# Optimization experiments

Hardware: AMD Instinct MI355X
Metric: run time of the kernel (lower is better)

The kernel has to match this reference:

```python
import jax, jax.numpy as jnp
import numpy as np

N = 100000      # nodes
E = 1000000     # edges (before self-loops)
IN_DIM = 256
H = 4           # heads
C = 32          # out_dim per head
NEG_SLOPE = 0.2  # PyG GATConv default negative_slope


def setup_inputs() -> dict:
    key = jax.random.key(0)
    ks = jax.random.split(key, 6)
    x = jax.random.normal(ks[0], (N, IN_DIM), jnp.float32)
    W = jax.random.normal(ks[1], (IN_DIM, H * C), jnp.float32) * (1.0 / np.sqrt(IN_DIM))
    a_src = jax.random.normal(ks[2], (H, C), jnp.float32) * 0.1
    a_dst = jax.random.normal(ks[3], (H, C), jnp.float32) * 0.1
    bias = jnp.zeros((H * C,), jnp.float32)
    edge_index = jax.random.randint(ks[4], (2, E), 0, N, dtype=jnp.int32)
    return {"x": x, "W": W, "a_src": a_src, "a_dst": a_dst, "bias": bias,
            "edge_index": edge_index}


def reference(x, W, a_src, a_dst, bias, edge_index):
    n = x.shape[0]
    # PyG GATConv default: add self-loops
    loops = jnp.arange(n, dtype=edge_index.dtype)
    src = jnp.concatenate([edge_index[0], loops])  # [E+N]
    dst = jnp.concatenate([edge_index[1], loops])  # [E+N]
    # linear transform -> [N, H, C]
    h = (x @ W).reshape(n, H, C)
    # per-node attention logits
    alpha_s = jnp.einsum('nhc,hc->nh', h, a_src)  # [N, H]
    alpha_d = jnp.einsum('nhc,hc->nh', h, a_dst)  # [N, H]
    # per-edge score, LeakyReLU
    e = jax.nn.leaky_relu(alpha_s[src] + alpha_d[dst], NEG_SLOPE)  # [E+N, H]
    # segment softmax over incoming edges of each destination node
    m = jax.lax.stop_gradient(jax.ops.segment_max(e, dst, num_segments=n))
    p = jnp.exp(e - m[dst])
    s = jax.ops.segment_sum(p, dst, num_segments=n)
    alpha = p / (s[dst] + 1e-16)  # [E+N, H]
    # weighted scatter-add of source features
    out = jax.ops.segment_sum(alpha[:, :, None] * h[src], dst, num_segments=n)  # [N, H, C]
    out = out.reshape(n, H * C) + bias
    return jnp.tanh(out)
```

## Files before the change

### kernel.cpp

```cpp
#include <hip/hip_runtime.h>

#define IN_DIM 256
#define HC     128
#define NHEAD  4
#define NEG    0.2f
#define BKT    1024
#define NBMAX  128
#define EPT2   8
#define BE     4096
#define PACKB  16

typedef __attribute__((ext_vector_type(8))) short short8v;
typedef __attribute__((ext_vector_type(4))) float f32x4;
typedef __attribute__((ext_vector_type(2))) float f32x2;
typedef __attribute__((ext_vector_type(4))) unsigned short ushort4v;

__device__ __forceinline__ unsigned short bf16_rn(float f) {
    unsigned u = __builtin_bit_cast(unsigned, f);
    return (unsigned short)((u + 0x7fffu + ((u >> 16) & 1u)) >> 16);
}
__device__ __forceinline__ float bf16_lo(unsigned v) {
    return __builtin_bit_cast(float, v << 16);
}
__device__ __forceinline__ float bf16_hi(unsigned v) {
    return __builtin_bit_cast(float, v & 0xffff0000u);
}
__device__ __forceinline__ float fast_tanh(float x) {
    float t = __expf(2.f * x);
    return fmaf(-2.f, __builtin_amdgcn_rcpf(t + 1.f), 1.f);
}
__device__ __forceinline__ float lrelu(float e) {
    return fmaxf(e, NEG * e);
}

__global__ __launch_bounds__(256) void pack_hist_kernel(const float* __restrict__ W,
                                                        unsigned short* __restrict__ w_hi,
                                                        const int* __restrict__ ei,
                                                        int* __restrict__ bucket_cnt,
                                                        int E, int nb) {
    __shared__ int lh[NBMAX];
    int tid = threadIdx.x;
    if (blockIdx.x < PACKB) {
        int t = blockIdx.x * 256 + tid;
        int l  = t & 63;
        int ct = (t >> 6) & 7;
        int s  = t >> 9;
        int kbase = s * 32 + (l >> 4) * 8;
        int col   = ct * 16 + (l & 15);
        size_t base = (size_t)t * 8;
#pragma unroll
        for (int e = 0; e < 8; ++e)
            w_hi[base + e] = bf16_rn(W[(size_t)(kbase + e) * HC + col]);
        return;
    }
    if (tid < NBMAX) lh[tid] = 0;
    __syncthreads();
    int base = (blockIdx.x - PACKB) * BE;
#pragma unroll
    for (int i = 0; i < 16; ++i) {
        int e = base + i * 256 + tid;
        if (e < E) atomicAdd(&lh[ei[E + e] >> 10], 1);
    }
    __syncthreads();
    if (tid < nb && lh[tid]) atomicAdd(&bucket_cnt[tid], lh[tid]);
}

__global__ __launch_bounds__(128) void bucket_scan_kernel(const int* __restrict__ bucket_cnt,
                                                          int* __restrict__ bucket_base,
                                                          int* __restrict__ bucket_cursor,
                                                          int nb) {
    __shared__ int ws0[1];
    int t = threadIdx.x;
    int v = (t < nb) ? bucket_cnt[t] : 0;
    int lane = t & 63, wd = t >> 6;
    int x = v;
#pragma unroll
    for (int off = 1; off < 64; off <<= 1) {
        int y = __shfl_up(x, off);
        if (lane >= off) x += y;
    }
    if (wd == 0 && lane == 63) ws0[0] = x;
    __syncthreads();
    int wo = wd ? ws0[0] : 0;
    int excl = wo + x - v;
    if (t < nb) { bucket_base[t] = excl; bucket_cursor[t] = excl; }
    if (t == 127) bucket_base[nb] = wo + x;
}

union KSmem {
    struct {
        unsigned short s_bf[64 * 256];
        float pS[64][4];
        float pD[64][4];
    } g;
    struct {
        int lh[NBMAX];
        int lofs[NBMAX];
        int gofs[NBMAX];
        int ws0;
        unsigned buf[BE];
    } s;
};

__global__ __launch_bounds__(512) void scatter_gemm_kernel(const int* __restrict__ ei,
                                                           int* __restrict__ bucket_cursor,
                                                           unsigned* __restrict__ bucket_data,
                                                           int E, int nb, int nblkE, int totalB,
                                                           const float* __restrict__ x,
                                                           const unsigned short* __restrict__ w_hi,
                                                           const float* __restrict__ a_src,
                                                           const float* __restrict__ a_dst,
                                                           unsigned short* __restrict__ h_bf,
                                                           float* __restrict__ alpha_s,
                                                           float* __restrict__ alpha_d, int n) {
    __shared__ KSmem sm;
    const int tid = threadIdx.x;
    const int bid = (int)blockIdx.x;

    const int s_before = (int)(((long long)bid * nblkE) / totalB);
    const bool is_scat = (int)(((long long)(bid + 1) * nblkE) / totalB) > s_before;

    if (is_scat) {
        if (tid < NBMAX) sm.s.lh[tid] = 0;
        __syncthreads();

        int base = s_before * BE;
        int bb[EPT2]; unsigned wv[EPT2]; int rr[EPT2];
#pragma unroll
        for (int i = 0; i < EPT2; ++i) {
            int e = base + i * 512 + tid;
            if (e < E) {
                int src = ei[e];
                int dst = ei[E + e];
                bb[i] = dst >> 10;
                wv[i] = (unsigned)src | ((unsigned)(dst & 1023) << 17);
                rr[i] = atomicAdd(&sm.s.lh[bb[i]], 1);
            } else bb[i] = -1;
        }
        __syncthreads();

        int lane = tid & 63, wd = tid >> 6;
        int v_ = 0, x_ = 0;
        if (tid < NBMAX) {
            v_ = sm.s.lh[tid]; x_ = v_;
#pragma unroll
            for (int off = 1; off < 64; off <<= 1) {
                int y = __shfl_up(x_, off);
                if (lane >= off) x_ += y;
            }
            if (wd == 0 && lane == 63) sm.s.ws0 = x_;
        }
        __syncthreads();
        if (tid < NBMAX) {
            int wo = wd ? sm.s.ws0 : 0;
            sm.s.lofs[tid] = wo + x_ - v_;
        }
        __syncthreads();

#pragma unroll
        for (int i = 0; i < EPT2; ++i)
            if (bb[i] >= 0) sm.s.buf[sm.s.lofs[bb[i]] + rr[i]] = wv[i];
        if (tid < nb) sm.s.gofs[tid] = sm.s.lh[tid] ? atomicAdd(&bucket_cursor[tid], sm.s.lh[tid]) : 0;
        __syncthreads();

        int wid = tid >> 6;
        for (int bk = wid; bk < nb; bk += 8) {
            int lo = sm.s.lofs[bk], cnt = sm.s.lh[bk], g = sm.s.gofs[bk];
            for (int j = lane; j < cnt; j += 64)
                bucket_data[g + j] = sm.s.buf[lo + j];
        }
        return;
    }

    const int gidx = bid - s_before;
    if (gidx * 64 >= n) return;
    const int l   = tid & 63;
    const int wv_ = tid >> 6;
    const int row0 = gidx * 64;

    const f32x4* x4 = reinterpret_cast<const f32x4*>(x);
#pragma unroll
    for (int i = 0; i < 8; ++i) {
        int row = i * 8 + wv_;
        int c4  = l;
        f32x4 v = (f32x4){0.f, 0.f, 0.f, 0.f};
        if (row0 + row < n) v = __builtin_nontemporal_load(&x4[(size_t)(row0 + row) * 64 + c4]);
        ushort4v b;
        b[0] = bf16_rn(v[0]); b[1] = bf16_rn(v[1]);
        b[2] = bf16_rn(v[2]); b[3] = bf16_rn(v[3]);
        int slot = (c4 >> 1) ^ (row & 7);
        int uidx = row * 256 + (slot << 3) + ((c4 & 1) << 2);
        *reinterpret_cast<ushort4v*>(&sm.g.s_bf[uidx]) = b;
    }
    __syncthreads();

    const int ct_g = wv_ & 3;
    const int rt_g = wv_ >> 2;
    const int rrow = l & 15;
    const int kq   = l >> 4;

    f32x4 acc[2][2];
#pragma unroll
    for (int a = 0; a < 2; ++a)
#pragma unroll
        for (int b = 0; b < 2; ++b) acc[a][b] = (f32x4){0.f, 0.f, 0.f, 0.f};

    for (int s = 0; s < 8; ++s) {
        short8v bh[2];
#pragma unroll
        for (int c = 0; c < 2; ++c) {
            int ct = ct_g * 2 + c;
            bh[c] = *reinterpret_cast<const short8v*>(w_hi + ((size_t)(s * 8 + ct) * 64 + l) * 8);
        }
#pragma unroll
        for (int r = 0; r < 2; ++r) {
            int arow = rt_g * 32 + r * 16 + rrow;
            int c16  = kq + s * 4;
            int uidx = arow * 256 + ((c16 ^ (arow & 7)) << 3);
            short8v ah = *reinterpret_cast<const short8v*>(&sm.g.s_bf[uidx]);
#pragma unroll
            for (int c = 0; c < 2; ++c)
                acc[r][c] = __builtin_amdgcn_mfma_f32_16x16x32_bf16(ah, bh[c], acc[r][c], 0, 0, 0);
        }
    }

#pragma unroll
    for (int r = 0; r < 2; ++r) {
#pragma unroll
        for (int c = 0; c < 2; ++c) {
            int col = (ct_g * 2 + c) * 16 + (l & 15);
#pragma unroll
            for (int q = 0; q < 4; ++q) {
                int row = row0 + rt_g * 32 + r * 16 + (l >> 4) * 4 + q;
                if (row < n) h_bf[(size_t)row * HC + col] = bf16_rn(acc[r][c][q]);
            }
        }
    }

    float asc[2], adc[2];
#pragma unroll
    for (int c = 0; c < 2; ++c) {
        int col = (ct_g * 2 + c) * 16 + (l & 15);
        asc[c] = a_src[col];
        adc[c] = a_dst[col];
    }
#pragma unroll
    for (int r = 0; r < 2; ++r) {
#pragma unroll
        for (int q = 0; q < 4; ++q) {
            float vS = acc[r][0][q] * asc[0] + acc[r][1][q] * asc[1];
            float vD = acc[r][0][q] * adc[0] + acc[r][1][q] * adc[1];
#pragma unroll
            for (int m = 1; m < 16; m <<= 1) {
                vS += __shfl_xor(vS, m);
                vD += __shfl_xor(vD, m);
            }
            if ((l & 15) == 0) {
                int rl = rt_g * 32 + r * 16 + (l >> 4) * 4 + q;
                sm.g.pS[rl][ct_g] = vS;
                sm.g.pD[rl][ct_g] = vD;
            }
        }
    }
    __syncthreads();
    if (tid < 256) {
        int rl = tid >> 2, h = tid & 3;
        int row = row0 + rl;
        if (row < n) {
            alpha_s[(size_t)row * 4 + h] = sm.g.pS[rl][h];
            alpha_d[(size_t)row * 4 + h] = sm.g.pD[rl][h];
        }
    }
}

__global__ __launch_bounds__(1024) void bucket_build_kernel(const int* __restrict__ bucket_base,
                                                            const unsigned* __restrict__ bucket_data,
                                                            int* __restrict__ deg,
                                                            int* __restrict__ row_start,
                                                            int* __restrict__ csr_src, int n) {
    __shared__ int lc[BKT];
    __shared__ int sc[BKT];
    __shared__ int wsum[16];

    int b = blockIdx.x;
    int base = bucket_base[b];
    int end  = bucket_base[b + 1];
    int t = threadIdx.x;

    lc[t] = 0;
    __syncthreads();
    for (int i = base + t; i < end; i += 1024)
        atomicAdd(&lc[__builtin_nontemporal_load(&bucket_data[i]) >> 17], 1);
    __syncthreads();

    int val = lc[t];
    int lane = t & 63, wd = t >> 6;
    int x = val;
#pragma unroll
    for (int off = 1; off < 64; off <<= 1) {
        int y = __shfl_up(x, off);
        if (lane >= off) x += y;
    }
    if (lane == 63) wsum[wd] = x;
    __syncthreads();
    if (wd == 0 && lane < 16) {
        int y = wsum[lane];
#pragma unroll
        for (int off = 1; off < 16; off <<= 1) {
            int z = __shfl_up(y, off);
            if (lane >= off) y += z;
        }
        wsum[lane] = y;
    }
    __syncthreads();
    int wo = wd ? wsum[wd - 1] : 0;
    int excl = wo + x - val;
    sc[t] = excl;
    int v = b * BKT + t;
    if (v < n) { deg[v] = val; row_start[v] = base + excl; }
    lc[t] = 0;
    __syncthreads();

    for (int i = base + t; i < end; i += 1024) {
        unsigned w = bucket_data[i];
        int d = w >> 17;
        int src = (int)(w & 0x1FFFFu);
        int p = atomicAdd(&lc[d], 1);
        csr_src[base + sc[d] + p] = src;
    }
}

__global__ __launch_bounds__(256, 4) void gather_kernel(const int* __restrict__ row_start,
                                                        const int* __restrict__ deg,
                                                        const int* __restrict__ csr_src,
                                                        const float* __restrict__ alpha_s,
                                                        const float* __restrict__ alpha_d,
                                                        const unsigned short* __restrict__ h_bf,
                                                        const float* __restrict__ bias,
                                                        float* __restrict__ out, int n) {
    int lane = threadIdx.x & 63;
    int wid  = threadIdx.x >> 6;
    int v = blockIdx.x * 4 + wid;
    if (v >= n) return;
    int start = row_start[v];
    int cnt = deg[v];
    int head = lane >> 4;
    int hc   = lane & 3;

    const unsigned* hb = reinterpret_cast<const unsigned*>(h_bf);

    float adC = alpha_d[(size_t)v * 4 + hc];
    float asC = alpha_s[(size_t)v * 4 + hc];
    float adH = __shfl(adC, head);
    float asH = __shfl(asC, head);
    float pself = __expf(lrelu(asH + adH));
    unsigned hv0 = hb[((unsigned)v << 6) + lane];
    float s = pself;
    float accx = pself * bf16_lo(hv0);
    float accy = pself * bf16_hi(hv0);

    int j = 0;
    for (; j + 8 <= cnt; j += 8) {
        int cv = csr_src[start + j + (lane & 7)];
        int sj = __shfl(cv, lane >> 2);
        float av = alpha_s[(size_t)sj * 4 + hc];
        float w  = __expf(lrelu(av + adC));
#pragma unroll
        for (int k = 0; k < 8; ++k) {
            int sk   = __shfl(cv, k);
            float wk = __shfl(w, (k << 2) | head);
            unsigned hk = hb[((unsigned)sk << 6) + lane];
            s += wk;
            accx = fmaf(wk, bf16_lo(hk), accx);
            accy = fmaf(wk, bf16_hi(hk), accy);
        }
    }
    if (j + 4 <= cnt) {
        int cv = csr_src[start + j + (lane & 3)];
        int sj = __shfl(cv, lane >> 2);
        float av = alpha_s[(size_t)sj * 4 + hc];
        float w  = __expf(lrelu(av + adC));
#pragma unroll
        for (int k = 0; k < 4; ++k) {
            int sk   = __shfl(cv, k);
            float wk = __shfl(w, (k << 2) | head);
            unsigned hk = hb[((unsigned)sk << 6) + lane];
            s += wk;
            accx = fmaf(wk, bf16_lo(hk), accx);
            accy = fmaf(wk, bf16_hi(hk), accy);
        }
        j += 4;
    }
    for (; j < cnt; ++j) {
        int s0 = csr_src[start + j];
        float a0 = alpha_s[(size_t)s0 * 4 + head];
        unsigned h0 = hb[((unsigned)s0 << 6) + lane];
        float w0 = __expf(lrelu(a0 + adH));
        s += w0;
        accx = fmaf(w0, bf16_lo(h0), accx);
        accy = fmaf(w0, bf16_hi(h0), accy);
    }

    float invH = __builtin_amdgcn_rcpf(s + 1e-16f);
    float2 b = reinterpret_cast<const float2*>(bias)[lane];
    f32x2 o;
    o[0] = fast_tanh(fmaf(accx, invH, b.x));
    o[1] = fast_tanh(fmaf(accy, invH, b.y));
    __builtin_nontemporal_store(o, &reinterpret_cast<f32x2*>(out)[(size_t)v * 64 + lane]);
}

extern "C" void kernel_launch(void* const* d_in, const int* in_sizes, int n_in,
                              void* d_out, int out_size, void* d_ws, size_t ws_size,
                              hipStream_t stream) {
    const float* x     = (const float*)d_in[0];
    const float* W     = (const float*)d_in[1];
    const float* a_src = (const float*)d_in[2];
    const float* a_dst = (const float*)d_in[3];
    const float* bias  = (const float*)d_in[4];
    const int*   ei    = (const int*)d_in[5];

    const int n = in_sizes[0] / IN_DIM;
    const int E = in_sizes[5] / 2;
    const int nb = (n + BKT - 1) / BKT;

    float* ws = (float*)d_ws;
    size_t off = 0;
    unsigned short* h_bf = (unsigned short*)(ws + off); off += (size_t)n * HC / 2;
    float* alpha_s = ws + off; off += (size_t)n * NHEAD;
    float* alpha_d = ws + off; off += (size_t)n * NHEAD;
    unsigned short* w_hi = (unsigned short*)(ws + off); off += 16384;
    int* ibase        = (int*)(ws + off);
    int* deg          = ibase;
    int* row_start    = ibase + n;
    int* bucket_cnt   = ibase + 2 * (size_t)n;
    int* bucket_base  = bucket_cnt + NBMAX;
    int* bucket_cursor= bucket_base + NBMAX + 1;
    unsigned* bucket_data = (unsigned*)(bucket_cursor + NBMAX);
    int* csr_src      = (int*)(bucket_data + E);

    float* out = (float*)d_out;

    const int nblkE = (E + BE - 1) / BE;
    const int gemmB = (n + 63) / 64;
    const int totalB = nblkE + gemmB;

    hipMemsetAsync(bucket_cnt, 0, NBMAX * sizeof(int), stream);

    pack_hist_kernel<<<PACKB + nblkE, 256, 0, stream>>>(W, w_hi, ei, bucket_cnt, E, nb);
    bucket_scan_kernel<<<1, 128, 0, stream>>>(bucket_cnt, bucket_base, bucket_cursor, nb);
    scatter_gemm_kernel<<<totalB, 512, 0, stream>>>(ei, bucket_cursor, bucket_data,
                                                    E, nb, nblkE, totalB,
                                                    x, w_hi, a_src, a_dst,
                                                    h_bf, alpha_s, alpha_d, n);
    bucket_build_kernel<<<nb, 1024, 0, stream>>>(bucket_base, bucket_data,
                                                 deg, row_start, csr_src, n);

    gather_kernel<<<(n + 3) / 4, 256, 0, stream>>>(row_start, deg, csr_src,
                                                   alpha_s, alpha_d, h_bf, bias, out, n);
}
```

Measured before the change: 134.9 us.

## Spread GEMM tiles across all CSR-build stages and halve bucket width

The node-feature GEMM used to be fused only into the scatter kernel. It is now split into fixed tile counts (GA/GB/GC and the remainder) that run inside the histogram, scan, scatter and bucket-build kernels, so every serial CSR stage has GEMM work to overlap with. W packing moves into its own small kernel. Buckets shrink to 512 nodes, giving twice as many buckets and 512-thread build blocks. The fixed split constants are tuned to this N and would misbehave if gemmB were smaller than their sum. The many tiny kernels each also pay larger launch and shared-memory footprints.

```diff
diff --git a/kernel.cpp b/kernel.cpp
--- a/kernel.cpp
+++ b/kernel.cpp
@@ -4,11 +4,14 @@
 #define HC     128
 #define NHEAD  4
 #define NEG    0.2f
-#define BKT    1024
-#define NBMAX  128
+#define BKT    512
+#define NBMAX  256
 #define EPT2   8
 #define BE     4096
 #define PACKB  16
+#define GA     400
+#define GB     150
+#define GC     600
 
 typedef __attribute__((ext_vector_type(8))) short short8v;
 typedef __attribute__((ext_vector_type(4))) float f32x4;
@@ -33,150 +36,30 @@
     return fmaxf(e, NEG * e);
 }
 
-__global__ __launch_bounds__(256) void pack_hist_kernel(const float* __restrict__ W,
-                                                        unsigned short* __restrict__ w_hi,
-                                                        const int* __restrict__ ei,
-                                                        int* __restrict__ bucket_cnt,
-                                                        int E, int nb) {
-    __shared__ int lh[NBMAX];
-    int tid = threadIdx.x;
-    if (blockIdx.x < PACKB) {
-        int t = blockIdx.x * 256 + tid;
-        int l  = t & 63;
-        int ct = (t >> 6) & 7;
-        int s  = t >> 9;
-        int kbase = s * 32 + (l >> 4) * 8;
-        int col   = ct * 16 + (l & 15);
-        size_t base = (size_t)t * 8;
-#pragma unroll
-        for (int e = 0; e < 8; ++e)
-            w_hi[base + e] = bf16_rn(W[(size_t)(kbase + e) * HC + col]);
-        return;
-    }
-    if (tid < NBMAX) lh[tid] = 0;
-    __syncthreads();
-    int base = (blockIdx.x - PACKB) * BE;
-#pragma unroll
-    for (int i = 0; i < 16; ++i) {
-        int e = base + i * 256 + tid;
-        if (e < E) atomicAdd(&lh[ei[E + e] >> 10], 1);
-    }
-    __syncthreads();
-    if (tid < nb && lh[tid]) atomicAdd(&bucket_cnt[tid], lh[tid]);
-}
-
-__global__ __launch_bounds__(128) void bucket_scan_kernel(const int* __restrict__ bucket_cnt,
-                                                          int* __restrict__ bucket_base,
-                                                          int* __restrict__ bucket_cursor,
-                                                          int nb) {
-    __shared__ int ws0[1];
-    int t = threadIdx.x;
-    int v = (t < nb) ? bucket_cnt[t] : 0;
-    int lane = t & 63, wd = t >> 6;
-    int x = v;
-#pragma unroll
-    for (int off = 1; off < 64; off <<= 1) {
-        int y = __shfl_up(x, off);
-        if (lane >= off) x += y;
-    }
-    if (wd == 0 && lane == 63) ws0[0] = x;
-    __syncthreads();
-    int wo = wd ? ws0[0] : 0;
-    int excl = wo + x - v;
-    if (t < nb) { bucket_base[t] = excl; bucket_cursor[t] = excl; }
-    if (t == 127) bucket_base[nb] = wo + x;
-}
-
-union KSmem {
-    struct {
-        unsigned short s_bf[64 * 256];
-        float pS[64][4];
-        float pD[64][4];
-    } g;
-    struct {
-        int lh[NBMAX];
-        int lofs[NBMAX];
-        int gofs[NBMAX];
-        int ws0;
-        unsigned buf[BE];
-    } s;
+struct GemmS {
+    unsigned short s_bf[64 * 256];
+    float pS[64][4];
+    float pD[64][4];
 };
-
-__global__ __launch_bounds__(512) void scatter_gemm_kernel(const int* __restrict__ ei,
-                                                           int* __restrict__ bucket_cursor,
-                                                           unsigned* __restrict__ bucket_data,
-                                                           int E, int nb, int nblkE, int totalB,
-                                                           const float* __restrict__ x,
-                                                           const unsigned short* __restrict__ w_hi,
-                                                           const float* __restrict__ a_src,
-                                                           const float* __restrict__ a_dst,
-                                                           unsigned short* __restrict__ h_bf,
-                                                           float* __restrict__ alpha_s,
-                                                           float* __restrict__ alpha_d, int n) {
-    __shared__ KSmem sm;
-    const int tid = threadIdx.x;
-    const int bid = (int)blockIdx.x;
-
-    const int s_before = (int)(((long long)bid * nblkE) / totalB);
-    const bool is_scat = (int)(((long long)(bid + 1) * nblkE) / totalB) > s_before;
-
-    if (is_scat) {
-        if (tid < NBMAX) sm.s.lh[tid] = 0;
-        __syncthreads();
-
-        int base = s_before * BE;
-        int bb[EPT2]; unsigned wv[EPT2]; int rr[EPT2];
-#pragma unroll
-        for (int i = 0; i < EPT2; ++i) {
-            int e = base + i * 512 + tid;
-            if (e < E) {
-                int src = ei[e];
-                int dst = ei[E + e];
-                bb[i] = dst >> 10;
-                wv[i] = (unsigned)src | ((unsigned)(dst & 1023) << 17);
-                rr[i] = atomicAdd(&sm.s.lh[bb[i]], 1);
-            } else bb[i] = -1;
-        }
-        __syncthreads();
-
-        int lane = tid & 63, wd = tid >> 6;
-        int v_ = 0, x_ = 0;
-        if (tid < NBMAX) {
-            v_ = sm.s.lh[tid]; x_ = v_;
-#pragma unroll
-            for (int off = 1; off < 64; off <<= 1) {
-                int y = __shfl_up(x_, off);
-                if (lane >= off) x_ += y;
-            }
-            if (wd == 0 && lane == 63) sm.s.ws0 = x_;
-        }
-        __syncthreads();
-        if (tid < NBMAX) {
-            int wo = wd ? sm.s.ws0 : 0;
-            sm.s.lofs[tid] = wo + x_ - v_;
-        }
-        __syncthreads();
-
-#pragma unroll
-        for (int i = 0; i < EPT2; ++i)
-            if (bb[i] >= 0) sm.s.buf[sm.s.lofs[bb[i]] + rr[i]] = wv[i];
-        if (tid < nb) sm.s.gofs[tid] = sm.s.lh[tid] ? atomicAdd(&bucket_cursor[tid], sm.s.lh[tid]) : 0;
-        __syncthreads();
-
-        int wid = tid >> 6;
-        for (int bk = wid; bk < nb; bk += 8) {
-            int lo = sm.s.lofs[bk], cnt = sm.s.lh[bk], g = sm.s.gofs[bk];
-            for (int j = lane; j < cnt; j += 64)
-                bucket_data[g + j] = sm.s.buf[lo + j];
-        }
-        return;
-    }
-
-    const int gidx = bid - s_before;
-    if (gidx * 64 >= n) return;
+union FusedS {
+    GemmS g;
+    struct { int lh[NBMAX]; } h;
+    struct { int ws[4]; } k2;
+    struct { int lh[NBMAX]; int lofs[NBMAX]; int gofs[NBMAX]; int ws[4];
+             unsigned buf[BE]; } s;
+    struct { int lc[BKT]; int sc[BKT]; int wsum[8]; } b;
+};
+
+__device__ __forceinline__ void gemm_body(GemmS& sm, int row0, int tid,
+                                          const float* __restrict__ x,
+                                          const unsigned short* __restrict__ w_hi,
+                                          const float* __restrict__ a_src,
+                                          const float* __restrict__ a_dst,
+                                          unsigned short* __restrict__ h_bf,
+                                          float* __restrict__ alpha_s,
+                                          float* __restrict__ alpha_d, int n) {
     const int l   = tid & 63;
     const int wv_ = tid >> 6;
-    const int row0 = gidx * 64;
 
     const f32x4* x4 = reinterpret_cast<const f32x4*>(x);
 #pragma unroll
@@ -190,7 +73,7 @@
         b[2] = bf16_rn(v[2]); b[3] = bf16_rn(v[3]);
         int slot = (c4 >> 1) ^ (row & 7);
         int uidx = row * 256 + (slot << 3) + ((c4 & 1) << 2);
-        *reinterpret_cast<ushort4v*>(&sm.g.s_bf[uidx]) = b;
+        *reinterpret_cast<ushort4v*>(&sm.s_bf[uidx]) = b;
     }
     __syncthreads();
 
@@ -203,7 +86,7 @@
 #pragma unroll
     for (int a = 0; a < 2; ++a)
 #pragma unroll
-        for (int b = 0; b < 2; ++b) acc[a][b] = (f32x4){0.f, 0.f, 0.f, 0.f};
+        for (int b2 = 0; b2 < 2; ++b2) acc[a][b2] = (f32x4){0.f, 0.f, 0.f, 0.f};
 
     for (int s = 0; s < 8; ++s) {
         short8v bh[2];
@@ -217,7 +100,7 @@
             int arow = rt_g * 32 + r * 16 + rrow;
             int c16  = kq + s * 4;
             int uidx = arow * 256 + ((c16 ^ (arow & 7)) << 3);
-            short8v ah = *reinterpret_cast<const short8v*>(&sm.g.s_bf[uidx]);
+            short8v ah = *reinterpret_cast<const short8v*>(&sm.s_bf[uidx]);
 #pragma unroll
             for (int c = 0; c < 2; ++c)
                 acc[r][c] = __builtin_amdgcn_mfma_f32_16x16x32_bf16(ah, bh[c], acc[r][c], 0, 0, 0);
@@ -257,8 +140,8 @@
             }
             if ((l & 15) == 0) {
                 int rl = rt_g * 32 + r * 16 + (l >> 4) * 4 + q;
-                sm.g.pS[rl][ct_g] = vS;
-                sm.g.pD[rl][ct_g] = vD;
+                sm.pS[rl][ct_g] = vS;
+                sm.pD[rl][ct_g] = vD;
             }
         }
     }
@@ -267,67 +150,238 @@
         int rl = tid >> 2, h = tid & 3;
         int row = row0 + rl;
         if (row < n) {
-            alpha_s[(size_t)row * 4 + h] = sm.g.pS[rl][h];
-            alpha_d[(size_t)row * 4 + h] = sm.g.pD[rl][h];
-        }
-    }
-}
-
-__global__ __launch_bounds__(1024) void bucket_build_kernel(const int* __restrict__ bucket_base,
-                                                            const unsigned* __restrict__ bucket_data,
-                                                            int* __restrict__ deg,
-                                                            int* __restrict__ row_start,
-                                                            int* __restrict__ csr_src, int n) {
-    __shared__ int lc[BKT];
-    __shared__ int sc[BKT];
-    __shared__ int wsum[16];
-
-    int b = blockIdx.x;
-    int base = bucket_base[b];
-    int end  = bucket_base[b + 1];
-    int t = threadIdx.x;
-
-    lc[t] = 0;
-    __syncthreads();
-    for (int i = base + t; i < end; i += 1024)
-        atomicAdd(&lc[__builtin_nontemporal_load(&bucket_data[i]) >> 17], 1);
-    __syncthreads();
-
-    int val = lc[t];
-    int lane = t & 63, wd = t >> 6;
-    int x = val;
-#pragma unroll
-    for (int off = 1; off < 64; off <<= 1) {
-        int y = __shfl_up(x, off);
-        if (lane >= off) x += y;
-    }
-    if (lane == 63) wsum[wd] = x;
-    __syncthreads();
-    if (wd == 0 && lane < 16) {
-        int y = wsum[lane];
-#pragma unroll
-        for (int off = 1; off < 16; off <<= 1) {
-            int z = __shfl_up(y, off);
-            if (lane >= off) y += z;
-        }
-        wsum[lane] = y;
-    }
-    __syncthreads();
-    int wo = wd ? wsum[wd - 1] : 0;
-    int excl = wo + x - val;
-    sc[t] = excl;
-    int v = b * BKT + t;
-    if (v < n) { deg[v] = val; row_start[v] = base + excl; }
-    lc[t] = 0;
-    __syncthreads();
-
-    for (int i = base + t; i < end; i += 1024) {
-        unsigned w = bucket_data[i];
-        int d = w >> 17;
-        int src = (int)(w & 0x1FFFFu);
-        int p = atomicAdd(&lc[d], 1);
-        csr_src[base + sc[d] + p] = src;
-    }
+            alpha_s[(size_t)row * 4 + h] = sm.pS[rl][h];
+            alpha_d[(size_t)row * 4 + h] = sm.pD[rl][h];
+        }
+    }
+}
+
+__global__ __launch_bounds__(256) void pack_w_kernel(const float* __restrict__ W,
+                                                     unsigned short* __restrict__ w_hi) {
+    int t = blockIdx.x * 256 + threadIdx.x;
+    if (t >= 8 * 8 * 64) return;
+    int l  = t & 63;
+    int ct = (t >> 6) & 7;
+    int s  = t >> 9;
+    int kbase = s * 32 + (l >> 4) * 8;
+    int col   = ct * 16 + (l & 15);
+    size_t base = (size_t)t * 8;
+#pragma unroll
+    for (int e = 0; e < 8; ++e)
+        w_hi[base + e] = bf16_rn(W[(size_t)(kbase + e) * HC + col]);
+}
+
+__global__ __launch_bounds__(512) void hist_gemm_kernel(const int* __restrict__ ei,
+                                                        int* __restrict__ bucket_cnt,
+                                                        int E, int nb, int nblkE,
+                                                        const float* __restrict__ x,
+                                                        const unsigned short* __restrict__ w_hi,
+                                                        const float* __restrict__ a_src,
+                                                        const float* __restrict__ a_dst,
+                                                        unsigned short* __restrict__ h_bf,
+                                                        float* __restrict__ alpha_s,
+                                                        float* __restrict__ alpha_d, int n) {
+    __shared__ FusedS sm;
+    int tid = threadIdx.x, bid = (int)blockIdx.x;
+    if (bid < nblkE) {
+        if (tid < NBMAX) sm.h.lh[tid] = 0;
+        __syncthreads();
+        int base = bid * BE;
+#pragma unroll
+        for (int i = 0; i < EPT2; ++i) {
+            int e = base + i * 512 + tid;
+            if (e < E) atomicAdd(&sm.h.lh[ei[E + e] >> 9], 1);
+        }
+        __syncthreads();
+        if (tid < nb && sm.h.lh[tid]) atomicAdd(&bucket_cnt[tid], sm.h.lh[tid]);
+        return;
+    }
+    int gidx = bid - nblkE;
+    if (gidx * 64 < n)
+        gemm_body(sm.g, gidx * 64, tid, x, w_hi, a_src, a_dst, h_bf, alpha_s, alpha_d, n);
+}
+
+__global__ __launch_bounds__(512) void scan_gemm_kernel(const int* __restrict__ bucket_cnt,
+                                                        int* __restrict__ bucket_base,
+                                                        int* __restrict__ bucket_cursor,
+                                                        int nb,
+                                                        const float* __restrict__ x,
+                                                        const unsigned short* __restrict__ w_hi,
+                                                        const float* __restrict__ a_src,
+                                                        const float* __restrict__ a_dst,
+                                                        unsigned short* __restrict__ h_bf,
+                                                        float* __restrict__ alpha_s,
+                                                        float* __restrict__ alpha_d, int n) {
+    __shared__ FusedS sm;
+    int tid = threadIdx.x, bid = (int)blockIdx.x;
+    if (bid == 0) {
+        int lane = tid & 63, wd = tid >> 6;
+        int v = 0, x_ = 0;
+        if (tid < 256) {
+            v = (tid < nb) ? bucket_cnt[tid] : 0;
+            x_ = v;
+#pragma unroll
+            for (int off = 1; off < 64; off <<= 1) {
+                int y = __shfl_up(x_, off);
+                if (lane >= off) x_ += y;
+            }
+            if (lane == 63) sm.k2.ws[wd] = x_;
+        }
+        __syncthreads();
+        if (tid == 0) {
+            int run = 0;
+#pragma unroll
+            for (int k = 0; k < 4; ++k) { int t2 = sm.k2.ws[k]; sm.k2.ws[k] = run; run += t2; }
+            bucket_base[nb] = run;
+        }
+        __syncthreads();
+        if (tid < nb) {
+            int excl = sm.k2.ws[wd] + x_ - v;
+            bucket_base[tid] = excl;
+            bucket_cursor[tid] = excl;
+        }
+        return;
+    }
+    int gidx = bid - 1 + GA;
+    if (gidx * 64 < n)
+        gemm_body(sm.g, gidx * 64, tid, x, w_hi, a_src, a_dst, h_bf, alpha_s, alpha_d, n);
+}
+
+__global__ __launch_bounds__(512) void scatter_gemm_kernel(const int* __restrict__ ei,
+                                                           int* __restrict__ bucket_cursor,
+                                                           unsigned* __restrict__ bucket_data,
+                                                           int E, int nb, int nblkE,
+                                                           const float* __restrict__ x,
+                                                           const unsigned short* __restrict__ w_hi,
+                                                           const float* __restrict__ a_src,
+                                                           const float* __restrict__ a_dst,
+                                                           unsigned short* __restrict__ h_bf,
+                                                           float* __restrict__ alpha_s,
+                                                           float* __restrict__ alpha_d, int n) {
+    __shared__ FusedS sm;
+    int tid = threadIdx.x, bid = (int)blockIdx.x;
+
+    if (bid < nblkE) {
+        if (tid < NBMAX) sm.s.lh[tid] = 0;
+        __syncthreads();
+
+        int base = bid * BE;
+        int bb[EPT2]; unsigned wv[EPT2]; int rr[EPT2];
+#pragma unroll
+        for (int i = 0; i < EPT2; ++i) {
+            int e = base + i * 512 + tid;
+            if (e < E) {
+                int src = ei[e];
+                int dst = ei[E + e];
+                bb[i] = dst >> 9;
+                wv[i] = (unsigned)src | ((unsigned)(dst & 511) << 17);
+                rr[i] = atomicAdd(&sm.s.lh[bb[i]], 1);
+            } else bb[i] = -1;
+        }
+        __syncthreads();
+
+        int lane = tid & 63, wd = tid >> 6;
+        int v_ = 0, x_ = 0;
+        if (tid < 256) {
+            v_ = sm.s.lh[tid]; x_ = v_;
+#pragma unroll
+            for (int off = 1; off < 64; off <<= 1) {
+                int y = __shfl_up(x_, off);
+                if (lane >= off) x_ += y;
+            }
+            if (lane == 63) sm.s.ws[wd] = x_;
+        }
+        __syncthreads();
+        if (tid == 0) {
+            int run = 0;
+#pragma unroll
+            for (int k = 0; k < 4; ++k) { int t2 = sm.s.ws[k]; sm.s.ws[k] = run; run += t2; }
+        }
+        __syncthreads();
+        if (tid < 256) sm.s.lofs[tid] = sm.s.ws[wd] + x_ - v_;
+        __syncthreads();
+
+#pragma unroll
+        for (int i = 0; i < EPT2; ++i)
+            if (bb[i] >= 0) sm.s.buf[sm.s.lofs[bb[i]] + rr[i]] = wv[i];
+        if (tid < nb) sm.s.gofs[tid] = sm.s.lh[tid] ? atomicAdd(&bucket_cursor[tid], sm.s.lh[tid]) : 0;
+        __syncthreads();
+
+        int wid = tid >> 6;
+        for (int bk = wid; bk < nb; bk += 8) {
+            int lo = sm.s.lofs[bk], cnt = sm.s.lh[bk], g = sm.s.gofs[bk];
+            for (int j = lane; j < cnt; j += 64)
+                bucket_data[g + j] = sm.s.buf[lo + j];
+        }
+        return;
+    }
+    int gidx = bid - nblkE + GA + GB;
+    if (gidx * 64 < n)
+        gemm_body(sm.g, gidx * 64, tid, x, w_hi, a_src, a_dst, h_bf, alpha_s, alpha_d, n);
+}
+
+__global__ __launch_bounds__(512) void build_gemm_kernel(const int* __restrict__ bucket_base,
+                                                         const unsigned* __restrict__ bucket_data,
+                                                         int* __restrict__ deg,
+                                                         int* __restrict__ row_start,
+                                                         int* __restrict__ csr_src,
+                                                         int nb,
+                                                         const float* __restrict__ x,
+                                                         const unsigned short* __restrict__ w_hi,
+                                                         const float* __restrict__ a_src,
+                                                         const float* __restrict__ a_dst,
+                                                         unsigned short* __restrict__ h_bf,
+                                                         float* __restrict__ alpha_s,
+                                                         float* __restrict__ alpha_d, int n) {
+    __shared__ FusedS sm;
+    int tid = threadIdx.x, bid = (int)blockIdx.x;
+
+    if (bid < nb) {
+        int base = bucket_base[bid];
+        int end  = bucket_base[bid + 1];
+        int t = tid;
+
+        sm.b.lc[t] = 0;
+        __syncthreads();
+        for (int i = base + t; i < end; i += 512)
+            atomicAdd(&sm.b.lc[__builtin_nontemporal_load(&bucket_data[i]) >> 17], 1);
+        __syncthreads();
+
+        int val = sm.b.lc[t];
+        int lane = t & 63, wd = t >> 6;
+        int x_ = val;
+#pragma unroll
+        for (int off = 1; off < 64; off <<= 1) {
+            int y = __shfl_up(x_, off);
+            if (lane >= off) x_ += y;
+        }
+        if (lane == 63) sm.b.wsum[wd] = x_;
+        __syncthreads();
+        if (t == 0) {
+            int run = 0;
+#pragma unroll
+            for (int k = 0; k < 8; ++k) { int t2 = sm.b.wsum[k]; sm.b.wsum[k] = run; run += t2; }
+        }
+        __syncthreads();
+        int excl = sm.b.wsum[wd] + x_ - val;
+        sm.b.sc[t] = excl;
+        int v = bid * BKT + t;
+        if (v < n) { deg[v] = val; row_start[v] = base + excl; }
+        sm.b.lc[t] = 0;
+        __syncthreads();
+
+        for (int i = base + t; i < end; i += 512) {
+            unsigned w = bucket_data[i];
+            int d = w >> 17;
+            int src = (int)(w & 0x1FFFFu);
+            int p = atomicAdd(&sm.b.lc[d], 1);
+            csr_src[base + sm.b.sc[d] + p] = src;
+        }
+        return;
+    }
+    int gidx = bid - nb + GA + GB + GC;
+    if (gidx * 64 < n)
+        gemm_body(sm.g, gidx * 64, tid, x, w_hi, a_src, a_dst, h_bf, alpha_s, alpha_d, n);
 }
 
 __global__ __launch_bounds__(256, 4) void gather_kernel(const int* __restrict__ row_start,
@@ -442,18 +496,25 @@
 
     const int nblkE = (E + BE - 1) / BE;
     const int gemmB = (n + 63) / 64;
-    const int totalB = nblkE + gemmB;
+    const int gD = gemmB - GA - GB - GC;
 
     hipMemsetAsync(bucket_cnt, 0, NBMAX * sizeof(int), stream);
 
-    pack_hist_kernel<<<PACKB + nblkE, 256, 0, stream>>>(W, w_hi, ei, bucket_cnt, E, nb);
-    bucket_scan_kernel<<<1, 128, 0, stream>>>(bucket_cnt, bucket_base, bucket_cursor, nb);
-    scatter_gemm_kernel<<<totalB, 512, 0, stream>>>(ei, bucket_cursor, bucket_data,
-                                                    E, nb, nblkE, totalB,
-                                                    x, w_hi, a_src, a_dst,
-                                                    h_bf, alpha_s, alpha_d, n);
-    bucket_build_kernel<<<nb, 1024, 0, stream>>>(bucket_base, bucket_data,
-                                                 deg, row_start, csr_src, n);
+    pack_w_kernel<<<PACKB, 256, 0, stream>>>(W, w_hi);
+    hist_gemm_kernel<<<nblkE + GA, 512, 0, stream>>>(ei, bucket_cnt, E, nb, nblkE,
+                                                     x, w_hi, a_src, a_dst,
+                                                     h_bf, alpha_s, alpha_d, n);
+    scan_gemm_kernel<<<1 + GB, 512, 0, stream>>>(bucket_cnt, bucket_base, bucket_cursor, nb,
+                                                 x, w_hi, a_src, a_dst,
+                                                 h_bf, alpha_s, alpha_d, n);
+    scatter_gemm_kernel<<<nblkE + GC, 512, 0, stream>>>(ei, bucket_cursor, bucket_data,
+                                                        E, nb, nblkE,
+                                                        x, w_hi, a_src, a_dst,
+                                                        h_bf, alpha_s, alpha_d, n);
+    build_gemm_kernel<<<nb + gD, 512, 0, stream>>>(bucket_base, bucket_data,
+                                                   deg, row_start, csr_src, nb,
+                                                   x, w_hi, a_src, a_dst,
+                                                   h_bf, alpha_s, alpha_d, n);
 
     gather_kernel<<<(n + 3) / 4, 256, 0, stream>>>(row_start, deg, csr_src,
                                                    alpha_s, alpha_d, h_bf, bias, out, n);
```

Result: slower. 144.8 us (+7.3%).

## Make GEMM blocks persistent with register-resident weights, group scatter blocks first

Applied to the files above, without the earlier changes.

The GEMM part of the fused scatter/GEMM kernel becomes a persistent grid of 512 blocks that loop over 64-row tiles. Each block loads all its W fragments into registers once instead of reloading them per tile. Scatter blocks are no longer interleaved with GEMM blocks; they now take the first block indices. The launch bound also requests 2 blocks per CU, and the bucket_build kernel drops its nontemporal load hint. The aim is to cut per-block weight reloads and launch overhead, at the cost of higher register pressure and less interleaving of scatter and GEMM work.

```diff
diff --git a/kernel.cpp b/kernel.cpp
--- a/kernel.cpp
+++ b/kernel.cpp
@@ -9,6 +9,7 @@
 #define EPT2   8
 #define BE     4096
 #define PACKB  16
+#define NGEMM  512
 
 typedef __attribute__((ext_vector_type(8))) short short8v;
 typedef __attribute__((ext_vector_type(4))) float f32x4;
@@ -102,29 +103,25 @@
     } s;
 };
 
-__global__ __launch_bounds__(512) void scatter_gemm_kernel(const int* __restrict__ ei,
-                                                           int* __restrict__ bucket_cursor,
-                                                           unsigned* __restrict__ bucket_data,
-                                                           int E, int nb, int nblkE, int totalB,
-                                                           const float* __restrict__ x,
-                                                           const unsigned short* __restrict__ w_hi,
-                                                           const float* __restrict__ a_src,
-                                                           const float* __restrict__ a_dst,
-                                                           unsigned short* __restrict__ h_bf,
-                                                           float* __restrict__ alpha_s,
-                                                           float* __restrict__ alpha_d, int n) {
+__global__ __launch_bounds__(512, 2) void scatter_gemm_kernel(const int* __restrict__ ei,
+                                                              int* __restrict__ bucket_cursor,
+                                                              unsigned* __restrict__ bucket_data,
+                                                              int E, int nb, int nblkE,
+                                                              const float* __restrict__ x,
+                                                              const unsigned short* __restrict__ w_hi,
+                                                              const float* __restrict__ a_src,
+                                                              const float* __restrict__ a_dst,
+                                                              unsigned short* __restrict__ h_bf,
+                                                              float* __restrict__ alpha_s,
+                                                              float* __restrict__ alpha_d, int n) {
     __shared__ KSmem sm;
     const int tid = threadIdx.x;
-    const int bid = (int)blockIdx.x;
-
-    const int s_before = (int)(((long long)bid * nblkE) / totalB);
-    const bool is_scat = (int)(((long long)(bid + 1) * nblkE) / totalB) > s_before;
-
-    if (is_scat) {
+
+    if ((int)blockIdx.x < nblkE) {
         if (tid < NBMAX) sm.s.lh[tid] = 0;
         __syncthreads();
 
-        int base = s_before * BE;
+        int base = blockIdx.x * BE;
         int bb[EPT2]; unsigned wv[EPT2]; int rr[EPT2];
 #pragma unroll
         for (int i = 0; i < EPT2; ++i) {
@@ -172,104 +169,109 @@
         return;
     }
 
-    const int gidx = bid - s_before;
-    if (gidx * 64 >= n) return;
     const int l   = tid & 63;
     const int wv_ = tid >> 6;
-    const int row0 = gidx * 64;
-
-    const f32x4* x4 = reinterpret_cast<const f32x4*>(x);
-#pragma unroll
-    for (int i = 0; i < 8; ++i) {
-        int row = i * 8 + wv_;
-        int c4  = l;
-        f32x4 v = (f32x4){0.f, 0.f, 0.f, 0.f};
-        if (row0 + row < n) v = __builtin_nontemporal_load(&x4[(size_t)(row0 + row) * 64 + c4]);
-        ushort4v b;
-        b[0] = bf16_rn(v[0]); b[1] = bf16_rn(v[1]);
-        b[2] = bf16_rn(v[2]); b[3] = bf16_rn(v[3]);
-        int slot = (c4 >> 1) ^ (row & 7);
-        int uidx = row * 256 + (slot << 3) + ((c4 & 1) << 2);
-        *reinterpret_cast<ushort4v*>(&sm.g.s_bf[uidx]) = b;
-    }
-    __syncthreads();
-
     const int ct_g = wv_ & 3;
     const int rt_g = wv_ >> 2;
     const int rrow = l & 15;
     const int kq   = l >> 4;
 
-    f32x4 acc[2][2];
-#pragma unroll
-    for (int a = 0; a < 2; ++a)
-#pragma unroll
-        for (int b = 0; b < 2; ++b) acc[a][b] = (f32x4){0.f, 0.f, 0.f, 0.f};
-
-    for (int s = 0; s < 8; ++s) {
-        short8v bh[2];
-#pragma unroll
-        for (int c = 0; c < 2; ++c) {
-            int ct = ct_g * 2 + c;
-            bh[c] = *reinterpret_cast<const short8v*>(w_hi + ((size_t)(s * 8 + ct) * 64 + l) * 8);
-        }
+    short8v bhall[8][2];
+#pragma unroll
+    for (int s = 0; s < 8; ++s)
+#pragma unroll
+        for (int c = 0; c < 2; ++c)
+            bhall[s][c] = *reinterpret_cast<const short8v*>(
+                w_hi + ((size_t)(s * 8 + ct_g * 2 + c) * 64 + l) * 8);
+
+    const f32x4* x4 = reinterpret_cast<const f32x4*>(x);
+
+    for (int gidx = (int)blockIdx.x - nblkE; gidx * 64 < n; gidx += NGEMM) {
+        const int row0 = gidx * 64;
+
+#pragma unroll
+        for (int i = 0; i < 8; ++i) {
+            int row = i * 8 + wv_;
+            int c4  = l;
+            f32x4 v = (f32x4){0.f, 0.f, 0.f, 0.f};
+            if (row0 + row < n) v = __builtin_nontemporal_load(&x4[(size_t)(row0 + row) * 64 + c4]);
+            ushort4v b;
+            b[0] = bf16_rn(v[0]); b[1] = bf16_rn(v[1]);
+            b[2] = bf16_rn(v[2]); b[3] = bf16_rn(v[3]);
+            int slot = (c4 >> 1) ^ (row & 7);
+            int uidx = row * 256 + (slot << 3) + ((c4 & 1) << 2);
+            *reinterpret_cast<ushort4v*>(&sm.g.s_bf[uidx]) = b;
+        }
+        __syncthreads();
+
+        f32x4 acc[2][2];
+#pragma unroll
+        for (int a = 0; a < 2; ++a)
+#pragma unroll
+            for (int b2 = 0; b2 < 2; ++b2) acc[a][b2] = (f32x4){0.f, 0.f, 0.f, 0.f};
+
+#pragma unroll
+        for (int s = 0; s < 8; ++s) {
+#pragma unroll
+            for (int r = 0; r < 2; ++r) {
+                int arow = rt_g * 32 + r * 16 + rrow;
+                int c16  = kq + s * 4;
+                int uidx = arow * 256 + ((c16 ^ (arow & 7)) << 3);
+                short8v ah = *reinterpret_cast<const short8v*>(&sm.g.s_bf[uidx]);
+#pragma unroll
+                for (int c = 0; c < 2; ++c)
+                    acc[r][c] = __builtin_amdgcn_mfma_f32_16x16x32_bf16(ah, bhall[s][c], acc[r][c], 0, 0, 0);
+            }
+        }
+
 #pragma unroll
         for (int r = 0; r < 2; ++r) {
-            int arow = rt_g * 32 + r * 16 + rrow;
-            int c16  = kq + s * 4;
-            int uidx = arow * 256 + ((c16 ^ (arow & 7)) << 3);
-            short8v ah = *reinterpret_cast<const short8v*>(&sm.g.s_bf[uidx]);
-#pragma unroll
-            for (int c = 0; c < 2; ++c)
-                acc[r][c] = __builtin_amdgcn_mfma_f32_16x16x32_bf16(ah, bh[c], acc[r][c], 0, 0, 0);
-        }
-    }
-
-#pragma unroll
-    for (int r = 0; r < 2; ++r) {
+#pragma unroll
+            for (int c = 0; c < 2; ++c) {
+                int col = (ct_g * 2 + c) * 16 + (l & 15);
+#pragma unroll
+                for (int q = 0; q < 4; ++q) {
+                    int row = row0 + rt_g * 32 + r * 16 + (l >> 4) * 4 + q;
+                    if (row < n) h_bf[(size_t)row * HC + col] = bf16_rn(acc[r][c][q]);
+                }
+            }
+        }
+
+        float asc[2], adc[2];
 #pragma unroll
         for (int c = 0; c < 2; ++c) {
             int col = (ct_g * 2 + c) * 16 + (l & 15);
+            asc[c] = a_src[col];
+            adc[c] = a_dst[col];
+        }
+#pragma unroll
+        for (int r = 0; r < 2; ++r) {
 #pragma unroll
             for (int q = 0; q < 4; ++q) {
-                int row = row0 + rt_g * 32 + r * 16 + (l >> 4) * 4 + q;
-                if (row < n) h_bf[(size_t)row * HC + col] = bf16_rn(acc[r][c][q]);
+                float vS = acc[r][0][q] * asc[0] + acc[r][1][q] * asc[1];
+                float vD = acc[r][0][q] * adc[0] + acc[r][1][q] * adc[1];
+#pragma unroll
+                for (int m = 1; m < 16; m <<= 1) {
+                    vS += __shfl_xor(vS, m);
+                    vD += __shfl_xor(vD, m);
+                }
+                if ((l & 15) == 0) {
+                    int rl = rt_g * 32 + r * 16 + (l >> 4) * 4 + q;
+                    sm.g.pS[rl][ct_g] = vS;
+                    sm.g.pD[rl][ct_g] = vD;
+                }
             }
         }
-    }
-
-    float asc[2], adc[2];
-#pragma unroll
-    for (int c = 0; c < 2; ++c) {
-        int col = (ct_g * 2 + c) * 16 + (l & 15);
-        asc[c] = a_src[col];
-        adc[c] = a_dst[col];
-    }
-#pragma unroll
-    for (int r = 0; r < 2; ++r) {
-#pragma unroll
-        for (int q = 0; q < 4; ++q) {
-            float vS = acc[r][0][q] * asc[0] + acc[r][1][q] * asc[1];
-            float vD = acc[r][0][q] * adc[0] + acc[r][1][q] * adc[1];
-#pragma unroll
-            for (int m = 1; m < 16; m <<= 1) {
-                vS += __shfl_xor(vS, m);
-                vD += __shfl_xor(vD, m);
+        __syncthreads();
+        if (tid < 256) {
+            int rl = tid >> 2, h = tid & 3;
+            int row = row0 + rl;
+            if (row < n) {
+                alpha_s[(size_t)row * 4 + h] = sm.g.pS[rl][h];
+                alpha_d[(size_t)row * 4 + h] = sm.g.pD[rl][h];
             }
-            if ((l & 15) == 0) {
-                int rl = rt_g * 32 + r * 16 + (l >> 4) * 4 + q;
-                sm.g.pS[rl][ct_g] = vS;
-                sm.g.pD[rl][ct_g] = vD;
-            }
-        }
-    }
-    __syncthreads();
-    if (tid < 256) {
-        int rl = tid >> 2, h = tid & 3;
-        int row = row0 + rl;
-        if (row < n) {
-            alpha_s[(size_t)row * 4 + h] = sm.g.pS[rl][h];
-            alpha_d[(size_t)row * 4 + h] = sm.g.pD[rl][h];
-        }
+        }
+        __syncthreads();
     }
 }
 
@@ -290,7 +292,7 @@
     lc[t] = 0;
     __syncthreads();
     for (int i = base + t; i < end; i += 1024)
-        atomicAdd(&lc[__builtin_nontemporal_load(&bucket_data[i]) >> 17], 1);
+        atomicAdd(&lc[bucket_data[i] >> 17], 1);
     __syncthreads();
 
     int val = lc[t];
@@ -441,17 +443,15 @@
     float* out = (float*)d_out;
 
     const int nblkE = (E + BE - 1) / BE;
-    const int gemmB = (n + 63) / 64;
-    const int totalB = nblkE + gemmB;
 
     hipMemsetAsync(bucket_cnt, 0, NBMAX * sizeof(int), stream);
 
     pack_hist_kernel<<<PACKB + nblkE, 256, 0, stream>>>(W, w_hi, ei, bucket_cnt, E, nb);
     bucket_scan_kernel<<<1, 128, 0, stream>>>(bucket_cnt, bucket_base, bucket_cursor, nb);
-    scatter_gemm_kernel<<<totalB, 512, 0, stream>>>(ei, bucket_cursor, bucket_data,
-                                                    E, nb, nblkE, totalB,
-                                                    x, w_hi, a_src, a_dst,
-                                                    h_bf, alpha_s, alpha_d, n);
+    scatter_gemm_kernel<<<nblkE + NGEMM, 512, 0, stream>>>(ei, bucket_cursor, bucket_data,
+                                                           E, nb, nblkE,
+                                                           x, w_hi, a_src, a_dst,
+                                                           h_bf, alpha_s, alpha_d, n);
     bucket_build_kernel<<<nb, 1024, 0, stream>>>(bucket_base, bucket_data,
                                                  deg, row_start, csr_src, n);
 
```

Result: slower. 144.8 us (+7.3%).
